# Performance work log

Measured on AMD Instinct MI355X. Metric: run time of the kernel, lower is better.

The kernel has to match this reference:

```python
import jax, jax.numpy as jnp
import numpy as np

N = 50000   # num nodes
C = 256     # in_channels
O = 256     # out_channels
D = 32      # fixed degree per node
S = 16      # num_samples


def setup_inputs() -> dict:
    key = jax.random.key(0)
    ks = jax.random.split(key, 8)
    w = 1.0 / np.sqrt(C).astype(np.float32)
    x = jax.random.normal(ks[0], (N, C), dtype=jnp.float32)
    neighbors = jax.random.randint(ks[1], (N, D), 0, N)  # padded adjacency (degree D for every node)
    W_self = jax.random.uniform(ks[2], (C, O), dtype=jnp.float32, minval=-w, maxval=w)
    b_self = jax.random.uniform(ks[3], (O,), dtype=jnp.float32, minval=-w, maxval=w)
    W_neigh = jax.random.uniform(ks[4], (C, O), dtype=jnp.float32, minval=-w, maxval=w)
    b_neigh = jax.random.uniform(ks[5], (O,), dtype=jnp.float32, minval=-w, maxval=w)
    W_coarsen = jax.random.uniform(ks[6], (C, O), dtype=jnp.float32, minval=-w, maxval=w)
    b_coarsen = jax.random.uniform(ks[7], (O,), dtype=jnp.float32, minval=-w, maxval=w)
    return dict(x=x, W_self=W_self, b_self=b_self, W_neigh=W_neigh, b_neigh=b_neigh,
                W_coarsen=W_coarsen, b_coarsen=b_coarsen, neighbors=neighbors)


def reference(x, W_self, b_self, W_neigh, b_neigh, W_coarsen, b_coarsen, neighbors):
    # Deterministic partition of each node's D neighbors into S sampled + (D-S) unsampled.
    sampled = neighbors[:, :S]     # [N, S]
    unsampled = neighbors[:, S:]   # [N, D-S]
    # Batched gather + mean aggregation (replaces the per-node Python loop).
    agg_s = jnp.mean(x[sampled], axis=1)    # [N, C]
    agg_u = jnp.mean(x[unsampled], axis=1)  # [N, C]
    # out[v] = W_self x[v] + W_neigh mean(sampled) + W_coarsen mean(unsampled) (+ biases)
    out = (x @ W_self + b_self) + (agg_s @ W_neigh + b_neigh) + (agg_u @ W_coarsen + b_coarsen)
    return out
```

## Files before the change

kernel.cpp:

```cpp
#include <hip/hip_runtime.h>
#include <stdint.h>
#include <stddef.h>


#define NN   50000
#define NPAD 50048
#define ODIM 256

typedef __bf16 bf16x8 __attribute__((ext_vector_type(8)));
typedef float  f32x4  __attribute__((ext_vector_type(4)));
typedef float  f32x2  __attribute__((ext_vector_type(2)));
typedef unsigned short u16x8 __attribute__((ext_vector_type(8)));
typedef unsigned short u16x4 __attribute__((ext_vector_type(4)));

static __device__ __forceinline__ unsigned short f2b(float f) {
    unsigned u = __builtin_bit_cast(unsigned, f);
    u += 0x7fffu + ((u >> 16) & 1u);
    return (unsigned short)(u >> 16);
}

__global__ void k_prep_w(const float* __restrict__ Wself, const float* __restrict__ bself,
                         const float* __restrict__ Wneigh, const float* __restrict__ bneigh,
                         const float* __restrict__ Wcoar, const float* __restrict__ bcoar,
                         unsigned short* __restrict__ Wb, float* __restrict__ bias) {
    int k = blockIdx.x;
    int n = threadIdx.x;
    const float* W = (k < 256) ? Wself : (k < 512) ? Wneigh : Wcoar;
    int kl = k & 255;
    float v = W[(size_t)kl * ODIM + n];
    int g = k >> 3;
    int j = k & 7;
    Wb[((size_t)g * ODIM + n) * 8 + j] = f2b(v);
    if (k == 0) bias[n] = bself[n] + bneigh[n] + bcoar[n];
}

__global__ void k_convert_x(const float* __restrict__ x, unsigned short* __restrict__ Ax,
                            unsigned char* __restrict__ X8) {
    int p = blockIdx.x * 256 + threadIdx.x;
    if (p >= NN * 32) return;
    int i  = p >> 5;
    int c8 = p & 31;
    const f32x4* src = (const f32x4*)(x + (size_t)i * 256 + c8 * 8);
    f32x4 v0 = src[0], v1 = src[1];
    u16x8 o;
    o[0] = f2b(v0[0]); o[1] = f2b(v0[1]); o[2] = f2b(v0[2]); o[3] = f2b(v0[3]);
    o[4] = f2b(v1[0]); o[5] = f2b(v1[1]); o[6] = f2b(v1[2]); o[7] = f2b(v1[3]);
    *(u16x8*)(Ax + ((size_t)c8 * NPAD + i) * 8) = o;
    unsigned d0 = __builtin_amdgcn_cvt_pk_fp8_f32(v0[0], v0[1], 0, false);
    d0 = (unsigned)__builtin_amdgcn_cvt_pk_fp8_f32(v0[2], v0[3], d0, true);
    unsigned d1 = __builtin_amdgcn_cvt_pk_fp8_f32(v1[0], v1[1], 0, false);
    d1 = (unsigned)__builtin_amdgcn_cvt_pk_fp8_f32(v1[2], v1[3], d1, true);
    uint2 o8; o8.x = d0; o8.y = d1;
    *(uint2*)(X8 + (size_t)i * 256 + c8 * 8) = o8;
}

__global__ __launch_bounds__(512) void k_gather(const int* __restrict__ nbr,
                                                const unsigned char* __restrict__ X8,
                                                unsigned short* __restrict__ Ax) {
    __shared__ unsigned short aggl[8][512];
    const int wid  = threadIdx.x >> 6;
    const int lane = threadIdx.x & 63;
    const int i = blockIdx.x * 8 + wid;
    const int* nb = nbr + (size_t)i * 32;
    float s0 = 0, s1 = 0, s2 = 0, s3 = 0, u0 = 0, u1 = 0, u2 = 0, u3 = 0;
#pragma unroll
    for (int j = 0; j < 32; ++j) {
        int idx = nb[j];
        unsigned d = *(const unsigned*)(X8 + (size_t)idx * 256 + lane * 4);
        f32x2 lo = __builtin_amdgcn_cvt_pk_f32_fp8(d, false);
        f32x2 hi = __builtin_amdgcn_cvt_pk_f32_fp8(d, true);
        if (j < 16) { s0 += lo[0]; s1 += lo[1]; s2 += hi[0]; s3 += hi[1]; }
        else        { u0 += lo[0]; u1 += lo[1]; u2 += hi[0]; u3 += hi[1]; }
    }
    const float rc = 1.0f / 16.0f;
    u16x4 os = { f2b(s0 * rc), f2b(s1 * rc), f2b(s2 * rc), f2b(s3 * rc) };
    u16x4 ou = { f2b(u0 * rc), f2b(u1 * rc), f2b(u2 * rc), f2b(u3 * rc) };
    *(u16x4*)&aggl[wid][lane * 4]       = os;
    *(u16x4*)&aggl[wid][256 + lane * 4] = ou;
    __syncthreads();
    const int tau = threadIdx.x;
    const int gl = tau >> 3, r = tau & 7;
    u16x8 v = *(const u16x8*)&aggl[r][gl * 8];
    *(u16x8*)(Ax + ((size_t)(32 + gl) * NPAD + blockIdx.x * 8 + r) * 8) = v;
}

#define BM 128
#define BN 128
#define BK 32
#define NT 24

__global__ __launch_bounds__(256, 3) void k_gemm(const unsigned short* __restrict__ Ax,
                                                 const unsigned short* __restrict__ Wb,
                                                 const float* __restrict__ bias,
                                                 float* __restrict__ out) {
    __shared__ __align__(16) unsigned short lds[3][2][4096];
    const int tid  = threadIdx.x;
    const int wid  = tid >> 6;
    const int lane = tid & 63;
    const int bid  = blockIdx.x;
    const int mt = bid >> 1, nt = bid & 1;
    const int row0 = mt * BM;
    const int n0   = nt * BN;
    const int wm = (wid >> 1) * 64, wn = (wid & 1) * 64;
    const int l15 = lane & 15, l4 = lane >> 4;

    f32x4 acc[4][4] = {};

    auto stage = [&](int buf, int t) {
#pragma unroll
        for (int q4 = 0; q4 < 4; ++q4) {
            const int q    = (wid & 1) * 4 + q4;
            const int kc   = q >> 1;
            const int half = q & 1;
            const int g    = t * 4 + kc;
            if (wid < 2) {
                const unsigned short* src =
                    Ax + ((size_t)g * NPAD + row0 + half * 64 + lane) * 8;
                unsigned short* dst = &lds[buf][0][kc * 1024 + half * 512];
                __builtin_amdgcn_global_load_lds(
                    (const __attribute__((address_space(1))) void*)src,
                    (__attribute__((address_space(3))) void*)dst, 16, 0, 0);
            } else {
                const unsigned short* src =
                    Wb + ((size_t)g * ODIM + n0 + half * 64 + lane) * 8;
                unsigned short* dst = &lds[buf][1][kc * 1024 + half * 512];
                __builtin_amdgcn_global_load_lds(
                    (const __attribute__((address_space(1))) void*)src,
                    (__attribute__((address_space(3))) void*)dst, 16, 0, 0);
            }
        }
    };

    stage(0, 0);
    stage(1, 1);
#pragma unroll
    for (int t = 0; t < NT; ++t) {
        if (t < NT - 1) asm volatile("s_waitcnt vmcnt(4)" ::: "memory");
        else            asm volatile("s_waitcnt vmcnt(0)" ::: "memory");
        __builtin_amdgcn_s_barrier();
        __builtin_amdgcn_sched_barrier(0);
        if (t + 2 < NT) stage((t + 2) % 3, t + 2);
        const int buf = t % 3;
        bf16x8 af[4], bfr[4];
#pragma unroll
        for (int mi = 0; mi < 4; ++mi)
            af[mi] = *(const bf16x8*)&lds[buf][0][l4 * 1024 + (wm + mi * 16 + l15) * 8];
#pragma unroll
        for (int ni = 0; ni < 4; ++ni)
            bfr[ni] = *(const bf16x8*)&lds[buf][1][l4 * 1024 + (wn + ni * 16 + l15) * 8];
#pragma unroll
        for (int mi = 0; mi < 4; ++mi)
#pragma unroll
            for (int ni = 0; ni < 4; ++ni)
                acc[mi][ni] = __builtin_amdgcn_mfma_f32_16x16x32_bf16(
                    af[mi], bfr[ni], acc[mi][ni], 0, 0, 0);
    }

#pragma unroll
    for (int mi = 0; mi < 4; ++mi) {
        const int row = row0 + wm + mi * 16 + l4 * 4;
#pragma unroll
        for (int ni = 0; ni < 4; ++ni) {
            const int col = n0 + wn + ni * 16 + l15;
            const float bb = bias[col];
            f32x4 v = acc[mi][ni];
#pragma unroll
            for (int r = 0; r < 4; ++r) {
                const int rr = row + r;
                if (rr < NN) out[(size_t)rr * ODIM + col] = v[r] + bb;
            }
        }
    }
}

extern "C" void kernel_launch(void* const* d_in, const int* in_sizes, int n_in,
                              void* d_out, int out_size, void* d_ws, size_t ws_size,
                              hipStream_t stream) {
    const float* x      = (const float*)d_in[0];
    const float* Wself  = (const float*)d_in[1];
    const float* bself  = (const float*)d_in[2];
    const float* Wneigh = (const float*)d_in[3];
    const float* bneigh = (const float*)d_in[4];
    const float* Wcoar  = (const float*)d_in[5];
    const float* bcoar  = (const float*)d_in[6];
    const int*   nbr    = (const int*)d_in[7];
    float* out = (float*)d_out;

    unsigned short* Ax   = (unsigned short*)d_ws;
    unsigned char*  X8   = (unsigned char*)(Ax + (size_t)96 * NPAD * 8);
    unsigned short* Wb   = (unsigned short*)(X8 + (size_t)NN * 256);
    float*          bias = (float*)(Wb + (size_t)96 * ODIM * 8);

    k_prep_w<<<768, 256, 0, stream>>>(Wself, bself, Wneigh, bneigh, Wcoar, bcoar, Wb, bias);
    k_convert_x<<<(NN * 32 + 255) / 256, 256, 0, stream>>>(x, Ax, X8);
    k_gather<<<NN / 8, 512, 0, stream>>>(nbr, X8, Ax);
    k_gemm<<<(NPAD / BM) * 2, 256, 0, stream>>>(Ax, Wb, bias, out);
}
```

Measured before the change: 119.6 us.

## Load GEMM operands directly from global into registers, drop LDS staging

```diff
diff --git a/kernel.cpp b/kernel.cpp
--- a/kernel.cpp
+++ b/kernel.cpp
@@ -4,7 +4,7 @@
 
 
 #define NN   50000
-#define NPAD 50048
+#define NPAD 50176
 #define ODIM 256
 
 typedef __bf16 bf16x8 __attribute__((ext_vector_type(8)));
@@ -84,76 +84,54 @@
     *(u16x8*)(Ax + ((size_t)(32 + gl) * NPAD + blockIdx.x * 8 + r) * 8) = v;
 }
 
-#define BM 128
-#define BN 128
-#define BK 32
 #define NT 24
 
-__global__ __launch_bounds__(256, 3) void k_gemm(const unsigned short* __restrict__ Ax,
+__global__ __launch_bounds__(256, 2) void k_gemm(const unsigned short* __restrict__ Ax,
                                                  const unsigned short* __restrict__ Wb,
                                                  const float* __restrict__ bias,
                                                  float* __restrict__ out) {
-    __shared__ __align__(16) unsigned short lds[3][2][4096];
     const int tid  = threadIdx.x;
     const int wid  = tid >> 6;
     const int lane = tid & 63;
-    const int bid  = blockIdx.x;
-    const int mt = bid >> 1, nt = bid & 1;
-    const int row0 = mt * BM;
-    const int n0   = nt * BN;
+    const int l15 = lane & 15, l4 = lane >> 4;
+
+    const int bid = blockIdx.x;
+    const int g16 = bid >> 4, r16 = bid & 15;
+    const int mt = g16 * 8 + (r16 & 7);
+    const int nt = r16 >> 3;
+    const int row0 = mt * 128;
+    const int n0   = nt * 128;
     const int wm = (wid >> 1) * 64, wn = (wid & 1) * 64;
-    const int l15 = lane & 15, l4 = lane >> 4;
 
     f32x4 acc[4][4] = {};
 
-    auto stage = [&](int buf, int t) {
+    auto loadA = [&](bf16x8* a, int t) {
+        const int g = t * 4 + l4;
 #pragma unroll
-        for (int q4 = 0; q4 < 4; ++q4) {
-            const int q    = (wid & 1) * 4 + q4;
-            const int kc   = q >> 1;
-            const int half = q & 1;
-            const int g    = t * 4 + kc;
-            if (wid < 2) {
-                const unsigned short* src =
-                    Ax + ((size_t)g * NPAD + row0 + half * 64 + lane) * 8;
-                unsigned short* dst = &lds[buf][0][kc * 1024 + half * 512];
-                __builtin_amdgcn_global_load_lds(
-                    (const __attribute__((address_space(1))) void*)src,
-                    (__attribute__((address_space(3))) void*)dst, 16, 0, 0);
-            } else {
-                const unsigned short* src =
-                    Wb + ((size_t)g * ODIM + n0 + half * 64 + lane) * 8;
-                unsigned short* dst = &lds[buf][1][kc * 1024 + half * 512];
-                __builtin_amdgcn_global_load_lds(
-                    (const __attribute__((address_space(1))) void*)src,
-                    (__attribute__((address_space(3))) void*)dst, 16, 0, 0);
-            }
-        }
+        for (int mi = 0; mi < 4; ++mi)
+            a[mi] = *(const bf16x8*)(Ax + ((size_t)g * NPAD + row0 + wm + mi * 16 + l15) * 8);
+    };
+    auto loadB = [&](bf16x8* b, int t) {
+        const int g = t * 4 + l4;
+#pragma unroll
+        for (int ni = 0; ni < 4; ++ni)
+            b[ni] = *(const bf16x8*)(Wb + ((size_t)g * ODIM + n0 + wn + ni * 16 + l15) * 8);
     };
 
-    stage(0, 0);
-    stage(1, 1);
+    bf16x8 As[3][4], Bs[3][4];
+    loadA(As[0], 0); loadB(Bs[0], 0);
+    loadA(As[1], 1); loadB(Bs[1], 1);
 #pragma unroll
     for (int t = 0; t < NT; ++t) {
-        if (t < NT - 1) asm volatile("s_waitcnt vmcnt(4)" ::: "memory");
-        else            asm volatile("s_waitcnt vmcnt(0)" ::: "memory");
-        __builtin_amdgcn_s_barrier();
-        __builtin_amdgcn_sched_barrier(0);
-        if (t + 2 < NT) stage((t + 2) % 3, t + 2);
-        const int buf = t % 3;
-        bf16x8 af[4], bfr[4];
-#pragma unroll
-        for (int mi = 0; mi < 4; ++mi)
-            af[mi] = *(const bf16x8*)&lds[buf][0][l4 * 1024 + (wm + mi * 16 + l15) * 8];
-#pragma unroll
-        for (int ni = 0; ni < 4; ++ni)
-            bfr[ni] = *(const bf16x8*)&lds[buf][1][l4 * 1024 + (wn + ni * 16 + l15) * 8];
+        if (t + 2 < NT) { loadA(As[(t + 2) % 3], t + 2); loadB(Bs[(t + 2) % 3], t + 2); }
+        bf16x8* a = As[t % 3];
+        bf16x8* b = Bs[t % 3];
 #pragma unroll
         for (int mi = 0; mi < 4; ++mi)
 #pragma unroll
             for (int ni = 0; ni < 4; ++ni)
                 acc[mi][ni] = __builtin_amdgcn_mfma_f32_16x16x32_bf16(
-                    af[mi], bfr[ni], acc[mi][ni], 0, 0, 0);
+                    a[mi], b[ni], acc[mi][ni], 0, 0, 0);
     }
 
 #pragma unroll
@@ -194,5 +172,5 @@
     k_prep_w<<<768, 256, 0, stream>>>(Wself, bself, Wneigh, bneigh, Wcoar, bcoar, Wb, bias);
     k_convert_x<<<(NN * 32 + 255) / 256, 256, 0, stream>>>(x, Ax, X8);
     k_gather<<<NN / 8, 512, 0, stream>>>(nbr, X8, Ax);
-    k_gemm<<<(NPAD / BM) * 2, 256, 0, stream>>>(Ax, Wb, bias, out);
+    k_gemm<<<784, 256, 0, stream>>>(Ax, Wb, bias, out);
 }
```

Measured after the change: 109.6 us. 1.09x faster.

## Widen GEMM tile to full 256 output columns with 512-thread blocks

Applied to the files above, without the earlier changes.

```diff
diff --git a/kernel.cpp b/kernel.cpp
--- a/kernel.cpp
+++ b/kernel.cpp
@@ -4,8 +4,9 @@
 
 
 #define NN   50000
-#define NPAD 50048
+#define NPAD 50176
 #define ODIM 256
+#define NTK  24
 
 typedef __bf16 bf16x8 __attribute__((ext_vector_type(8)));
 typedef float  f32x4  __attribute__((ext_vector_type(4)));
@@ -84,46 +85,40 @@
     *(u16x8*)(Ax + ((size_t)(32 + gl) * NPAD + blockIdx.x * 8 + r) * 8) = v;
 }
 
-#define BM 128
-#define BN 128
-#define BK 32
-#define NT 24
-
-__global__ __launch_bounds__(256, 3) void k_gemm(const unsigned short* __restrict__ Ax,
+__global__ __launch_bounds__(512, 4) void k_gemm(const unsigned short* __restrict__ Ax,
                                                  const unsigned short* __restrict__ Wb,
                                                  const float* __restrict__ bias,
                                                  float* __restrict__ out) {
-    __shared__ __align__(16) unsigned short lds[3][2][4096];
+    __shared__ __align__(16) unsigned short lds[3][12288];
     const int tid  = threadIdx.x;
     const int wid  = tid >> 6;
     const int lane = tid & 63;
-    const int bid  = blockIdx.x;
-    const int mt = bid >> 1, nt = bid & 1;
-    const int row0 = mt * BM;
-    const int n0   = nt * BN;
-    const int wm = (wid >> 1) * 64, wn = (wid & 1) * 64;
     const int l15 = lane & 15, l4 = lane >> 4;
+    const int row0 = blockIdx.x * 128;
+    const int wr = wid >> 2, wc = wid & 3;
 
     f32x4 acc[4][4] = {};
 
     auto stage = [&](int buf, int t) {
 #pragma unroll
-        for (int q4 = 0; q4 < 4; ++q4) {
-            const int q    = (wid & 1) * 4 + q4;
-            const int kc   = q >> 1;
-            const int half = q & 1;
-            const int g    = t * 4 + kc;
-            if (wid < 2) {
+        for (int i = 0; i < 3; ++i) {
+            const int u = wid * 3 + i;
+            if (u < 8) {
+                const int kc = u >> 1, half = u & 1;
+                const int g  = t * 4 + kc;
                 const unsigned short* src =
                     Ax + ((size_t)g * NPAD + row0 + half * 64 + lane) * 8;
-                unsigned short* dst = &lds[buf][0][kc * 1024 + half * 512];
+                unsigned short* dst = &lds[buf][kc * 1024 + half * 512];
                 __builtin_amdgcn_global_load_lds(
                     (const __attribute__((address_space(1))) void*)src,
                     (__attribute__((address_space(3))) void*)dst, 16, 0, 0);
             } else {
+                const int v = u - 8;
+                const int kc = v >> 2, nq = v & 3;
+                const int g  = t * 4 + kc;
                 const unsigned short* src =
-                    Wb + ((size_t)g * ODIM + n0 + half * 64 + lane) * 8;
-                unsigned short* dst = &lds[buf][1][kc * 1024 + half * 512];
+                    Wb + ((size_t)g * ODIM + nq * 64 + lane) * 8;
+                unsigned short* dst = &lds[buf][4096 + kc * 2048 + nq * 512];
                 __builtin_amdgcn_global_load_lds(
                     (const __attribute__((address_space(1))) void*)src,
                     (__attribute__((address_space(3))) void*)dst, 16, 0, 0);
@@ -134,20 +129,20 @@
     stage(0, 0);
     stage(1, 1);
 #pragma unroll
-    for (int t = 0; t < NT; ++t) {
-        if (t < NT - 1) asm volatile("s_waitcnt vmcnt(4)" ::: "memory");
+    for (int t = 0; t < NTK; ++t) {
+        if (t < NTK - 1) asm volatile("s_waitcnt vmcnt(3)" ::: "memory");
         else            asm volatile("s_waitcnt vmcnt(0)" ::: "memory");
         __builtin_amdgcn_s_barrier();
         __builtin_amdgcn_sched_barrier(0);
-        if (t + 2 < NT) stage((t + 2) % 3, t + 2);
+        if (t + 2 < NTK) stage((t + 2) % 3, t + 2);
         const int buf = t % 3;
         bf16x8 af[4], bfr[4];
 #pragma unroll
         for (int mi = 0; mi < 4; ++mi)
-            af[mi] = *(const bf16x8*)&lds[buf][0][l4 * 1024 + (wm + mi * 16 + l15) * 8];
+            af[mi] = *(const bf16x8*)&lds[buf][l4 * 1024 + (wr * 64 + mi * 16 + l15) * 8];
 #pragma unroll
         for (int ni = 0; ni < 4; ++ni)
-            bfr[ni] = *(const bf16x8*)&lds[buf][1][l4 * 1024 + (wn + ni * 16 + l15) * 8];
+            bfr[ni] = *(const bf16x8*)&lds[buf][4096 + l4 * 2048 + (wc * 64 + ni * 16 + l15) * 8];
 #pragma unroll
         for (int mi = 0; mi < 4; ++mi)
 #pragma unroll
@@ -158,10 +153,10 @@
 
 #pragma unroll
     for (int mi = 0; mi < 4; ++mi) {
-        const int row = row0 + wm + mi * 16 + l4 * 4;
+        const int row = row0 + wr * 64 + mi * 16 + l4 * 4;
 #pragma unroll
         for (int ni = 0; ni < 4; ++ni) {
-            const int col = n0 + wn + ni * 16 + l15;
+            const int col = wc * 64 + ni * 16 + l15;
             const float bb = bias[col];
             f32x4 v = acc[mi][ni];
 #pragma unroll
@@ -194,5 +189,5 @@
     k_prep_w<<<768, 256, 0, stream>>>(Wself, bself, Wneigh, bneigh, Wcoar, bcoar, Wb, bias);
     k_convert_x<<<(NN * 32 + 255) / 256, 256, 0, stream>>>(x, Ax, X8);
     k_gather<<<NN / 8, 512, 0, stream>>>(nbr, X8, Ax);
-    k_gemm<<<(NPAD / BM) * 2, 256, 0, stream>>>(Ax, Wb, bias, out);
+    k_gemm<<<NPAD / 128, 512, 0, stream>>>(Ax, Wb, bias, out);
 }
```

After: 105.4 us. 11.9% less time.
